# Performance work log

Hardware: AMD Instinct MI355X
Metric: run time of the kernel (lower is better)

## Reference

```python
import jax, jax.numpy as jnp
import numpy as np

D = 128      # feature dim
H = 8        # heads
DH = D // H  # dim per head
N = 100000   # nodes
E = 600000   # edges
BN_EPS = 1e-5


def _bn(x, g, b, m, v):
    # BatchNorm1d in eval mode (running stats)
    return (x - m) * jax.lax.rsqrt(v + BN_EPS) * g + b


def setup_inputs() -> dict:
    key = jax.random.key(0)
    ks = jax.random.split(key, 32)
    s = 1.0 / np.sqrt(D)
    inp = {
        "x": jax.random.normal(ks[0], (N, D), jnp.float32),
        "edge_index": jax.random.randint(ks[1], (2, E), 0, N, jnp.int64),
        # type embeddings (1 node type, 1 edge type)
        "nt_emb": jax.random.normal(ks[2], (1, D), jnp.float32),
        "et_emb": jax.random.normal(ks[3], (1, D), jnp.float32),
        # merge_node_edge_attr: Linear(2D,D) -> BN -> ReLU -> Linear(D,D)
        "mW1": jax.random.normal(ks[4], (2 * D, D), jnp.float32) * s,
        "mb1": jnp.zeros((D,), jnp.float32),
        "m_g": jnp.ones((D,), jnp.float32),
        "m_b": jnp.zeros((D,), jnp.float32),
        "m_m": jax.random.normal(ks[5], (D,), jnp.float32) * 0.1,
        "m_v": jax.random.uniform(ks[6], (D,), jnp.float32, 0.5, 1.5),
        "mW2": jax.random.normal(ks[7], (D, D), jnp.float32) * s,
        "mb2": jnp.zeros((D,), jnp.float32),
        # residual projection (no bias)
        "resW": jax.random.normal(ks[8], (D, D), jnp.float32) * s,
        # attention projections
        "qW": jax.random.normal(ks[9], (D, D), jnp.float32) * s,
        "qb": jnp.zeros((D,), jnp.float32),
        "kW": jax.random.normal(ks[10], (D, D), jnp.float32) * s,
        "kb": jnp.zeros((D,), jnp.float32),
        "vW": jax.random.normal(ks[11], (D, D), jnp.float32) * s,
        "vb": jnp.zeros((D,), jnp.float32),
        # output mlp: Linear -> BN -> LeakyReLU -> Linear
        "oW1": jax.random.normal(ks[12], (D, D), jnp.float32) * s,
        "ob1": jnp.zeros((D,), jnp.float32),
        "o_g": jnp.ones((D,), jnp.float32),
        "o_b": jnp.zeros((D,), jnp.float32),
        "o_m": jax.random.normal(ks[13], (D,), jnp.float32) * 0.1,
        "o_v": jax.random.uniform(ks[14], (D,), jnp.float32, 0.5, 1.5),
        "oW2": jax.random.normal(ks[15], (D, D), jnp.float32) * s,
        "ob2": jnp.zeros((D,), jnp.float32),
    }
    return inp


def reference(x, edge_index, nt_emb, et_emb, mW1, mb1, m_g, m_b, m_m, m_v, mW2, mb2,
              resW, qW, qb, kW, kb, vW, vb, oW1, ob1, o_g, o_b, o_m, o_v, oW2, ob2):
    src = edge_index[0]
    dst = edge_index[1]
    n_nodes = x.shape[0]
    e = edge_index.shape[1]

    # GraphNodeEdgeAttr: edge attrs are constant per edge type; with one node
    # type, edge_attr[0] == edge_attr[1] == merge(cat[node_emb, edge_emb]).
    merged = jnp.concatenate([nt_emb[0], et_emb[0]])          # [2D]
    h = jax.nn.relu(_bn(merged @ mW1 + mb1, m_g, m_b, m_m, m_v))
    ea = h @ mW2 + mb2                                        # [D], broadcasts per edge

    # edge_update: per-edge multi-head attention scores
    x_j = x[src]                                              # [E, D] source feats
    x_i = x[dst]                                              # [E, D] target feats
    q = ((x_j + ea) @ qW + qb).reshape(e, H, DH) / jnp.sqrt(jnp.float32(DH))
    k = ((x_i + ea) @ kW + kb).reshape(e, H, DH)
    msg = (x_j @ vW + vb).reshape(e, H, DH)
    scores = jnp.sum(q * k, axis=2)                           # [E, H]

    # segment softmax keyed by source node index
    smax = jax.ops.segment_max(scores, src, num_segments=n_nodes)
    ex = jnp.exp(scores - smax[src])
    ssum = jax.ops.segment_sum(ex, src, num_segments=n_nodes)
    alpha = ex / ssum[src]                                    # [E, H]

    # message + scatter-add aggregation to destination nodes
    weighted = (msg * alpha[:, :, None]).reshape(e, H * DH)   # [E, D]
    aggr = jax.ops.segment_sum(weighted, dst, num_segments=n_nodes)  # [N, D]

    res = x @ resW
    z = aggr + res
    out = jax.nn.leaky_relu(_bn(z @ oW1 + ob1, o_g, o_b, o_m, o_v)) @ oW2 + ob2
    return out
```

## Files before the change

### kernel.cpp

```cpp
#include <hip/hip_runtime.h>

#define BN_EPS 1e-5f
#define SCAN_CHUNK 1024
#define BM 128
#define ZSTRIDE 132

typedef __attribute__((ext_vector_type(8))) short s16x8;
typedef __attribute__((ext_vector_type(4))) float f32x4;

__global__ __launch_bounds__(128) void k_ea(
    const float* __restrict__ nt, const float* __restrict__ et,
    const float* __restrict__ mW1, const float* __restrict__ mb1,
    const float* __restrict__ m_g, const float* __restrict__ m_b,
    const float* __restrict__ m_m, const float* __restrict__ m_v,
    const float* __restrict__ mW2, const float* __restrict__ mb2,
    const float* __restrict__ qW, const float* __restrict__ qb,
    const float* __restrict__ kW, const float* __restrict__ kb,
    float* __restrict__ eaq, float* __restrict__ eak)
{
    __shared__ float merged[256];
    __shared__ float h[128];
    __shared__ float sea[128];
    const int t = threadIdx.x;
    merged[t]       = nt[t];
    merged[128 + t] = et[t];
    __syncthreads();
    float acc = mb1[t];
    for (int i = 0; i < 256; ++i) acc = fmaf(merged[i], mW1[i * 128 + t], acc);
    acc = (acc - m_m[t]) * rsqrtf(m_v[t] + BN_EPS) * m_g[t] + m_b[t];
    h[t] = acc > 0.f ? acc : 0.f;
    __syncthreads();
    float acc2 = mb2[t];
    for (int k = 0; k < 128; ++k) acc2 = fmaf(h[k], mW2[k * 128 + t], acc2);
    sea[t] = acc2;
    __syncthreads();
    float aq = qb[t], ak = kb[t];
    for (int k = 0; k < 128; ++k) {
        const float e = sea[k];
        aq = fmaf(e, qW[k * 128 + t], aq);
        ak = fmaf(e, kW[k * 128 + t], ak);
    }
    eaq[t] = aq;
    eak[t] = ak;
}

__device__ __forceinline__ void split_store(float w, ushort* __restrict__ base,
                                            int j, int k)
{
    unsigned u = __builtin_bit_cast(unsigned, w);
    unsigned hi = (u + 0x7fffu + ((u >> 16) & 1u)) >> 16;
    float hif = __builtin_bit_cast(float, hi << 16);
    float res = w - hif;
    unsigned lo = __builtin_bit_cast(unsigned, res) >> 16;
    base[j * 128 + k]         = (ushort)hi;
    base[16384 + j * 128 + k] = (ushort)lo;
}

__global__ __launch_bounds__(128) void k_prep3(
    const float* __restrict__ W0, const float* __restrict__ W1,
    const float* __restrict__ W2, ushort* __restrict__ P)
{
    const int j = blockIdx.x;
    const int m = blockIdx.y;
    const int k = threadIdx.x;
    const float* W = (m == 0) ? W0 : (m == 1) ? W1 : W2;
    split_store(W[k * 128 + j], P + (size_t)m * 32768, j, k);
}

__global__ __launch_bounds__(128) void k_prep_out(
    const float* __restrict__ resW, const float* __restrict__ oW1,
    const float* __restrict__ oW2, ushort* __restrict__ P)
{
    __shared__ float col[128];
    const int j = blockIdx.x;
    const int m = blockIdx.y;
    const int k = threadIdx.x;
    float w;
    if (m == 0) {
        col[k] = oW1[k * 128 + j];
        __syncthreads();
        float acc = 0.f;
        for (int i = 0; i < 128; ++i) acc = fmaf(resW[k * 128 + i], col[i], acc);
        w = acc;
    } else {
        const float* W = (m == 1) ? oW1 : oW2;
        w = W[k * 128 + j];
    }
    split_store(w, P + (size_t)m * 32768, j, k);
}

template <int NT>
__device__ __forceinline__ void stage_w(const ushort* __restrict__ wpl,
                                        ushort* __restrict__ sw, int tid)
{
    const uint4* src = (const uint4*)wpl;
#pragma unroll
    for (int it = 0; it < 4096 / NT; ++it) {
        const int idx = it * NT + tid;
        const uint4 v = src[idx];
        const int plane = idx >> 11;
        const int rr = (idx >> 4) & 127;
        const int cb = (idx & 15) << 4;
        const int byteoff = ((rr * 256 + cb) ^ ((rr & 7) << 4));
        *(uint4*)((char*)sw + plane * 32768 + byteoff) = v;
    }
}

template <int CT>
__device__ __forceinline__ void mm_core(const float* __restrict__ Arow,
                                        const ushort* __restrict__ sw,
                                        int g, int r16, int ct0, f32x4* acc)
{
#pragma unroll
    for (int ks = 0; ks < 4; ++ks) {
        const float* ap = Arow + ks * 32 + g * 8;
        const float4 a0 = *(const float4*)(ap);
        const float4 a1 = *(const float4*)(ap + 4);
        float av[8] = {a0.x, a0.y, a0.z, a0.w, a1.x, a1.y, a1.z, a1.w};
        s16x8 ahi, alo;
#pragma unroll
        for (int j = 0; j < 8; ++j) {
            const unsigned u = __builtin_bit_cast(unsigned, av[j]);
            ahi[j] = (short)(u >> 16);
            const float hif = __builtin_bit_cast(float, u & 0xffff0000u);
            const float res = av[j] - hif;
            alo[j] = (short)(__builtin_bit_cast(unsigned, res) >> 16);
        }
        const int koff = ks * 64 + g * 16;
#pragma unroll
        for (int ct = 0; ct < CT; ++ct) {
            const int row = (ct0 + ct) * 16 + r16;
            const int byteoff = ((row * 256 + koff) ^ ((row & 7) << 4));
            const s16x8 bhi = *(const s16x8*)((const char*)sw + byteoff);
            const s16x8 blo = *(const s16x8*)((const char*)sw + 32768 + byteoff);
            acc[ct] = __builtin_amdgcn_mfma_f32_16x16x32_bf16(ahi, bhi, acc[ct], 0, 0, 0);
            acc[ct] = __builtin_amdgcn_mfma_f32_16x16x32_bf16(ahi, blo, acc[ct], 0, 0, 0);
            acc[ct] = __builtin_amdgcn_mfma_f32_16x16x32_bf16(alo, bhi, acc[ct], 0, 0, 0);
        }
    }
}

__global__ __launch_bounds__(512, 4) void k_mm_qkv(
    const float* __restrict__ x, const ushort* __restrict__ planes,
    const float* __restrict__ eaq, const float* __restrict__ eak,
    const float* __restrict__ vb,
    float* __restrict__ Q, float* __restrict__ K, float* __restrict__ V, int N)
{
    __shared__ ushort sw[2 * 128 * 128];
    const int tid = threadIdx.x;
    const int sel = blockIdx.y;
    stage_w<512>(planes + (size_t)sel * 32768, sw, tid);
    __syncthreads();

    const int wave = tid >> 6, lane = tid & 63;
    const int g = lane >> 4, r16 = lane & 15;
    const int n0 = blockIdx.x * BM + wave * 16;
    int nA = n0 + r16; if (nA >= N) nA = N - 1;

    f32x4 acc[8];
#pragma unroll
    for (int ct = 0; ct < 8; ++ct) acc[ct] = (f32x4){0.f, 0.f, 0.f, 0.f};
    mm_core<8>(x + (size_t)nA * 128, sw, g, r16, 0, acc);

    const float* bias = (sel == 0) ? eaq : (sel == 1) ? eak : vb;
    float* O          = (sel == 0) ? Q   : (sel == 1) ? K   : V;
    const float scale = (sel == 0) ? 0.25f : 1.0f;
#pragma unroll
    for (int ct = 0; ct < 8; ++ct) {
        const int c = ct * 16 + r16;
        const float bc = bias[c];
#pragma unroll
        for (int r = 0; r < 4; ++r) {
            const int n = n0 + g * 4 + r;
            if (n < N) O[(size_t)n * 128 + c] = (acc[ct][r] + bc) * scale;
        }
    }
}

__global__ __launch_bounds__(1024, 4) void k_out2(
    const float* __restrict__ x, const ushort* __restrict__ Po,
    const float* __restrict__ aggr,
    const float* __restrict__ ob1,
    const float* __restrict__ o_m, const float* __restrict__ o_v,
    const float* __restrict__ o_g, const float* __restrict__ o_b,
    const float* __restrict__ ob2,
    float* __restrict__ out, int N)
{
    __shared__ ushort sw[2 * 128 * 128];
    __shared__ float  tb[128 * ZSTRIDE];
    const int tid = threadIdx.x;
    const int wave = tid >> 6, lane = tid & 63;
    const int g = lane >> 4, r16 = lane & 15;
    const int wr = wave & 7, wc = wave >> 3;
    const int ct0 = wc * 4;
    const int n0 = blockIdx.x * BM;
    const int arow = wr * 16 + r16;
    int nA = n0 + arow; if (nA >= N) nA = N - 1;

    f32x4 acc[4];
#pragma unroll
    for (int ct = 0; ct < 4; ++ct) acc[ct] = (f32x4){0.f, 0.f, 0.f, 0.f};

    stage_w<1024>(Po, sw, tid);
    __syncthreads();
    mm_core<4>(x + (size_t)nA * 128, sw, g, r16, ct0, acc);
    __syncthreads();

    stage_w<1024>(Po + 32768, sw, tid);
    __syncthreads();
    mm_core<4>(aggr + (size_t)nA * 128, sw, g, r16, ct0, acc);
    __syncthreads();

#pragma unroll
    for (int ct = 0; ct < 4; ++ct) {
        const int c = (ct0 + ct) * 16 + r16;
        const float bc = ob1[c];
        const float rs = rsqrtf(o_v[c] + BN_EPS);
        const float mm = o_m[c], gg = o_g[c], bb = o_b[c];
#pragma unroll
        for (int r = 0; r < 4; ++r) {
            const int nrel = wr * 16 + g * 4 + r;
            float u = acc[ct][r] + bc;
            u = (u - mm) * rs * gg + bb;
            u = u > 0.f ? u : 0.01f * u;
            tb[nrel * ZSTRIDE + c] = u;
        }
    }
    stage_w<1024>(Po + 65536, sw, tid);
    __syncthreads();

#pragma unroll
    for (int ct = 0; ct < 4; ++ct) acc[ct] = (f32x4){0.f, 0.f, 0.f, 0.f};
    mm_core<4>(tb + arow * ZSTRIDE, sw, g, r16, ct0, acc);
#pragma unroll
    for (int ct = 0; ct < 4; ++ct) {
        const int c = (ct0 + ct) * 16 + r16;
        const float bc = ob2[c];
#pragma unroll
        for (int r = 0; r < 4; ++r) {
            const int n = n0 + wr * 16 + g * 4 + r;
            if (n < N) out[(size_t)n * 128 + c] = acc[ct][r] + bc;
        }
    }
}

__global__ __launch_bounds__(256) void k_edge1(
    const int* __restrict__ ei, const float* __restrict__ Q,
    const float* __restrict__ K, const int* __restrict__ epos,
    float* __restrict__ exp_, float* __restrict__ ssum, int E)
{
    const int t = blockIdx.x * 256 + threadIdx.x;
    const int e = t >> 3;
    if (e >= E) return;
    const int h = t & 7;
    const int s = ei[e];
    const int d = ei[E + e];
    const float* qp = Q + (size_t)s * 128 + h * 16;
    const float* kp = K + (size_t)d * 128 + h * 16;
    float acc = 0.f;
#pragma unroll
    for (int r = 0; r < 4; ++r) {
        const float4 a = *(const float4*)(qp + r * 4);
        const float4 b = *(const float4*)(kp + r * 4);
        acc += a.x * b.x + a.y * b.y + a.z * b.z + a.w * b.w;
    }
    const float v = __expf(acc);
    exp_[(size_t)epos[e] * 8 + h] = v;
    unsafeAtomicAdd(&ssum[(size_t)s * 8 + h], v);
}

__global__ __launch_bounds__(256) void k_vscale(
    float* __restrict__ V, const float* __restrict__ ssum, int N)
{
    const int i = blockIdx.x * 256 + threadIdx.x;
    if (i >= N * 32) return;
    const int row = i >> 5, q = i & 31, h = q >> 2;
    const float r = 1.0f / ssum[(size_t)row * 8 + h];
    float4 v = *(float4*)(V + (size_t)i * 4);
    v.x *= r; v.y *= r; v.z *= r; v.w *= r;
    *(float4*)(V + (size_t)i * 4) = v;
}

__global__ __launch_bounds__(256) void k_hist(const int* __restrict__ ei,
                                              int* __restrict__ deg, int E)
{
    const int e = blockIdx.x * 256 + threadIdx.x;
    if (e < E) atomicAdd(&deg[ei[E + e]], 1);
}

__global__ __launch_bounds__(256) void k_scan_partial(const int* __restrict__ deg,
                                                      int* __restrict__ part, int N)
{
    __shared__ int sd[256];
    const int b = blockIdx.x, t = threadIdx.x;
    const int base = b * SCAN_CHUNK + t * 4;
    int s = 0;
#pragma unroll
    for (int i = 0; i < 4; ++i) { const int idx = base + i; if (idx < N) s += deg[idx]; }
    sd[t] = s; __syncthreads();
    for (int off = 128; off > 0; off >>= 1) {
        if (t < off) sd[t] += sd[t + off];
        __syncthreads();
    }
    if (t == 0) part[b] = sd[0];
}

__global__ __launch_bounds__(256) void k_scan_top(int* __restrict__ part, int nb)
{
    __shared__ int sd[256];
    const int t = threadIdx.x;
    const int orig = (t < nb) ? part[t] : 0;
    sd[t] = orig;
    __syncthreads();
    for (int off = 1; off < 256; off <<= 1) {
        const int v = (t >= off) ? sd[t - off] : 0;
        __syncthreads();
        sd[t] += v;
        __syncthreads();
    }
    if (t < nb) part[t] = sd[t] - orig;
}

__global__ __launch_bounds__(256) void k_scan_final(const int* __restrict__ deg,
                                                    const int* __restrict__ part,
                                                    int* __restrict__ row_start,
                                                    int* __restrict__ cursor, int N)
{
    __shared__ int ts[256];
    const int b = blockIdx.x, t = threadIdx.x;
    const int base = b * SCAN_CHUNK + t * 4;
    int v[4]; int s = 0;
#pragma unroll
    for (int i = 0; i < 4; ++i) { const int idx = base + i; v[i] = (idx < N) ? deg[idx] : 0; s += v[i]; }
    ts[t] = s; __syncthreads();
    for (int off = 1; off < 256; off <<= 1) {
        const int vv = (t >= off) ? ts[t - off] : 0;
        __syncthreads();
        ts[t] += vv;
        __syncthreads();
    }
    int run = part[b] + ((t > 0) ? ts[t - 1] : 0);
#pragma unroll
    for (int i = 0; i < 4; ++i) {
        const int idx = base + i;
        if (idx < N) { row_start[idx] = run; cursor[idx] = run; run += v[i]; }
    }
}

__global__ __launch_bounds__(256) void k_scatter(const int* __restrict__ ei,
                                                 int* __restrict__ cursor,
                                                 int* __restrict__ epos,
                                                 int* __restrict__ esrc, int E)
{
    const int e = blockIdx.x * 256 + threadIdx.x;
    if (e < E) {
        const int pos = atomicAdd(&cursor[ei[E + e]], 1);
        epos[e] = pos;
        esrc[pos] = ei[e];
    }
}

__global__ __launch_bounds__(256) void k_aggr(
    const int* __restrict__ esrc, const int* __restrict__ row_start,
    const int* __restrict__ deg, const float* __restrict__ V,
    const float* __restrict__ exp_, float* __restrict__ aggr, int N)
{
    const int tid = threadIdx.x;
    const int n = blockIdx.x * 4 + (tid >> 6);
    if (n >= N) return;
    const int lane = tid & 63;
    const int sub = lane >> 5;
    const int l = lane & 31;
    const int h = l >> 2;
    const int c0 = l * 4;
    const int rs = row_start[n];
    const int dg = deg[n];
    float4 acc = make_float4(0.f, 0.f, 0.f, 0.f);
    for (int j = sub; j < dg; j += 2) {
        const int idx = rs + j;
        const int s = esrc[idx];
        const float a = exp_[(size_t)idx * 8 + h];
        const float4 v = *(const float4*)(V + (size_t)s * 128 + c0);
        acc.x = fmaf(v.x, a, acc.x);
        acc.y = fmaf(v.y, a, acc.y);
        acc.z = fmaf(v.z, a, acc.z);
        acc.w = fmaf(v.w, a, acc.w);
    }
    acc.x += __shfl_xor(acc.x, 32, 64);
    acc.y += __shfl_xor(acc.y, 32, 64);
    acc.z += __shfl_xor(acc.z, 32, 64);
    acc.w += __shfl_xor(acc.w, 32, 64);
    if (sub == 0) *(float4*)(aggr + (size_t)n * 128 + c0) = acc;
}

extern "C" void kernel_launch(void* const* d_in, const int* in_sizes, int n_in,
                              void* d_out, int out_size, void* d_ws, size_t ws_size,
                              hipStream_t stream)
{
    const float* x    = (const float*)d_in[0];
    const int*   ei   = (const int*)d_in[1];
    const float* nt   = (const float*)d_in[2];
    const float* et   = (const float*)d_in[3];
    const float* mW1  = (const float*)d_in[4];
    const float* mb1  = (const float*)d_in[5];
    const float* m_g  = (const float*)d_in[6];
    const float* m_b  = (const float*)d_in[7];
    const float* m_m  = (const float*)d_in[8];
    const float* m_v  = (const float*)d_in[9];
    const float* mW2  = (const float*)d_in[10];
    const float* mb2  = (const float*)d_in[11];
    const float* resW = (const float*)d_in[12];
    const float* qW   = (const float*)d_in[13];
    const float* qb   = (const float*)d_in[14];
    const float* kW   = (const float*)d_in[15];
    const float* kb   = (const float*)d_in[16];
    const float* vW   = (const float*)d_in[17];
    const float* vb   = (const float*)d_in[18];
    const float* oW1  = (const float*)d_in[19];
    const float* ob1  = (const float*)d_in[20];
    const float* o_g  = (const float*)d_in[21];
    const float* o_b  = (const float*)d_in[22];
    const float* o_m  = (const float*)d_in[23];
    const float* o_v  = (const float*)d_in[24];
    const float* oW2  = (const float*)d_in[25];
    const float* ob2  = (const float*)d_in[26];
    float* out = (float*)d_out;

    const int N = in_sizes[0] / 128;
    const int E = in_sizes[1] / 2;

    float* ws   = (float*)d_ws;
    float* eaq  = ws;
    float* eak  = ws + 128;
    float* Q    = ws + 256;
    float* K    = Q + (size_t)N * 128;
    float* V    = K + (size_t)N * 128;
    float* exp_ = V + (size_t)N * 128;
    float* ssum = exp_ + (size_t)E * 8;
    int* deg       = (int*)(ssum + (size_t)N * 8);
    int* row_start = deg + N;
    int* cursor    = row_start + N;
    int* part      = cursor + N;
    int* epos      = part + 256;
    int* esrc      = epos + E;
    float* aggr = Q;
    ushort* Pq = (ushort*)ssum;
    ushort* Po = (ushort*)exp_;

    const int nbm  = (N + BM - 1) / BM;
    const int nbsc = (N + SCAN_CHUNK - 1) / SCAN_CHUNK;

    k_prep3<<<dim3(128, 3), 128, 0, stream>>>(qW, kW, vW, Pq);
    k_ea<<<1, 128, 0, stream>>>(nt, et, mW1, mb1, m_g, m_b, m_m, m_v, mW2, mb2,
                                qW, qb, kW, kb, eaq, eak);
    k_mm_qkv<<<dim3(nbm, 3), 512, 0, stream>>>(x, Pq, eaq, eak, vb, Q, K, V, N);

    hipMemsetAsync(ssum, 0, (size_t)N * 8 * sizeof(float), stream);
    hipMemsetAsync(deg, 0, (size_t)N * sizeof(int), stream);

    k_hist<<<(E + 255) / 256, 256, 0, stream>>>(ei, deg, E);
    k_scan_partial<<<nbsc, 256, 0, stream>>>(deg, part, N);
    k_scan_top<<<1, 256, 0, stream>>>(part, nbsc);
    k_scan_final<<<nbsc, 256, 0, stream>>>(deg, part, row_start, cursor, N);
    k_scatter<<<(E + 255) / 256, 256, 0, stream>>>(ei, cursor, epos, esrc, E);

    k_edge1<<<(int)(((size_t)E * 8 + 255) / 256), 256, 0, stream>>>(ei, Q, K, epos, exp_, ssum, E);
    k_vscale<<<(N * 32 + 255) / 256, 256, 0, stream>>>(V, ssum, N);
    k_aggr<<<(N + 3) / 4, 256, 0, stream>>>(esrc, row_start, deg, V, exp_, aggr, N);

    k_prep_out<<<dim3(128, 3), 128, 0, stream>>>(resW, oW1, oW2, Po);
    k_out2<<<nbm, 1024, 0, stream>>>(x, Po, aggr, ob1, o_m, o_v, o_g, o_b, ob2, out, N);
}
```

Before: 529.3 us.

## Compute edge attention scores by iterating destination-sorted CSR instead of raw edges

```diff
diff --git a/kernel.cpp b/kernel.cpp
--- a/kernel.cpp
+++ b/kernel.cpp
@@ -244,29 +244,36 @@
     }
 }
 
-__global__ __launch_bounds__(256) void k_edge1(
-    const int* __restrict__ ei, const float* __restrict__ Q,
-    const float* __restrict__ K, const int* __restrict__ epos,
-    float* __restrict__ exp_, float* __restrict__ ssum, int E)
-{
-    const int t = blockIdx.x * 256 + threadIdx.x;
-    const int e = t >> 3;
-    if (e >= E) return;
-    const int h = t & 7;
-    const int s = ei[e];
-    const int d = ei[E + e];
-    const float* qp = Q + (size_t)s * 128 + h * 16;
-    const float* kp = K + (size_t)d * 128 + h * 16;
-    float acc = 0.f;
-#pragma unroll
-    for (int r = 0; r < 4; ++r) {
-        const float4 a = *(const float4*)(qp + r * 4);
-        const float4 b = *(const float4*)(kp + r * 4);
-        acc += a.x * b.x + a.y * b.y + a.z * b.z + a.w * b.w;
-    }
-    const float v = __expf(acc);
-    exp_[(size_t)epos[e] * 8 + h] = v;
-    unsafeAtomicAdd(&ssum[(size_t)s * 8 + h], v);
+__global__ __launch_bounds__(256) void k_edge1csr(
+    const int* __restrict__ esrc, const int* __restrict__ row_start,
+    const int* __restrict__ deg, const float* __restrict__ Q,
+    const float* __restrict__ K, float* __restrict__ exp_,
+    float* __restrict__ ssum, int N)
+{
+    const int tid = threadIdx.x;
+    const int n = blockIdx.x * 4 + (tid >> 6);
+    if (n >= N) return;
+    const int lane = tid & 63;
+    const int sub = lane >> 5;
+    const int l = lane & 31;
+    const int h = l >> 2;
+    const int c0 = l * 4;
+    const int rs = row_start[n];
+    const int dg = deg[n];
+    const float4 kreg = *(const float4*)(K + (size_t)n * 128 + c0);
+    for (int j = sub; j < dg; j += 2) {
+        const int idx = rs + j;
+        const int s = esrc[idx];
+        const float4 q = *(const float4*)(Q + (size_t)s * 128 + c0);
+        float p = q.x * kreg.x + q.y * kreg.y + q.z * kreg.z + q.w * kreg.w;
+        p += __shfl_xor(p, 1, 64);
+        p += __shfl_xor(p, 2, 64);
+        if ((l & 3) == 0) {
+            const float v = __expf(p);
+            exp_[(size_t)idx * 8 + h] = v;
+            unsafeAtomicAdd(&ssum[(size_t)s * 8 + h], v);
+        }
+    }
 }
 
 __global__ __launch_bounds__(256) void k_vscale(
@@ -349,13 +356,11 @@
 
 __global__ __launch_bounds__(256) void k_scatter(const int* __restrict__ ei,
                                                  int* __restrict__ cursor,
-                                                 int* __restrict__ epos,
                                                  int* __restrict__ esrc, int E)
 {
     const int e = blockIdx.x * 256 + threadIdx.x;
     if (e < E) {
         const int pos = atomicAdd(&cursor[ei[E + e]], 1);
-        epos[e] = pos;
         esrc[pos] = ei[e];
     }
 }
@@ -441,8 +446,7 @@
     int* row_start = deg + N;
     int* cursor    = row_start + N;
     int* part      = cursor + N;
-    int* epos      = part + 256;
-    int* esrc      = epos + E;
+    int* esrc      = part + 256;
     float* aggr = Q;
     ushort* Pq = (ushort*)ssum;
     ushort* Po = (ushort*)exp_;
@@ -462,9 +466,9 @@
     k_scan_partial<<<nbsc, 256, 0, stream>>>(deg, part, N);
     k_scan_top<<<1, 256, 0, stream>>>(part, nbsc);
     k_scan_final<<<nbsc, 256, 0, stream>>>(deg, part, row_start, cursor, N);
-    k_scatter<<<(E + 255) / 256, 256, 0, stream>>>(ei, cursor, epos, esrc, E);
-
-    k_edge1<<<(int)(((size_t)E * 8 + 255) / 256), 256, 0, stream>>>(ei, Q, K, epos, exp_, ssum, E);
+    k_scatter<<<(E + 255) / 256, 256, 0, stream>>>(ei, cursor, esrc, E);
+
+    k_edge1csr<<<(N + 3) / 4, 256, 0, stream>>>(esrc, row_start, deg, Q, K, exp_, ssum, N);
     k_vscale<<<(N * 32 + 255) / 256, 256, 0, stream>>>(V, ssum, N);
     k_aggr<<<(N + 3) / 4, 256, 0, stream>>>(esrc, row_start, deg, V, exp_, aggr, N);
 
```

Result: faster. 496.9 us (-6.1%).
